# Kernel tuning notes

Measured on AMD Instinct MI355X. Metric: run time of the kernel, lower is better.

Reference implementation:

```python
import jax, jax.numpy as jnp
import numpy as np

DT = 0.1  # Euler timestep (init kwarg)

def setup_inputs() -> dict:
    key = jax.random.key(0)
    ks = jax.random.split(key, 6)
    B, L, S, U, H = 1024, 512, 64, 32, 512
    return {
        "initial_state": jax.random.normal(ks[0], (B, S), dtype=jnp.float32),
        "control_inputs": jax.random.normal(ks[1], (B, L, U), dtype=jnp.float32),
        "W1": jax.random.normal(ks[2], (S + U, H), dtype=jnp.float32) * (1.0 / np.sqrt(S + U)),
        "b1": jnp.zeros((H,), dtype=jnp.float32),
        "W2": jax.random.normal(ks[3], (H, S), dtype=jnp.float32) * (1.0 / np.sqrt(H)),
        "b2": jnp.zeros((S,), dtype=jnp.float32),
    }

def reference(initial_state, control_inputs, W1, b1, W2, b2):
    # Euler integration: state_{t+1} = state_t + dt * f(state_t, u_t)
    # f is a 2-layer tanh MLP on the concatenated [state, control].
    def step(state, u):
        z = jnp.concatenate([state, u], axis=-1)        # (B, S+U)
        diff = jnp.tanh(z @ W1 + b1) @ W2 + b2          # (B, S)
        new_state = state + diff * DT
        return new_state, new_state

    u_seq = jnp.swapaxes(control_inputs, 0, 1)          # (L, B, U)
    _, states = jax.lax.scan(step, initial_state, u_seq)  # (L, B, S)
    return jnp.swapaxes(states, 0, 1)                   # (B, L, S)
```

## Files before the change

kernel.cpp:

```cpp
#include <hip/hip_runtime.h>
#include <hip/hip_fp16.h>


typedef _Float16 f16;
typedef __attribute__((ext_vector_type(2))) _Float16 f16x2;
typedef __attribute__((ext_vector_type(8))) _Float16 f16x8;
typedef __attribute__((ext_vector_type(2))) float f32x2;
typedef __attribute__((ext_vector_type(4))) float f32x4;

#define MFMA16(a, b, c) __builtin_amdgcn_mfma_f32_16x16x32_f16((a), (b), (c), 0, 0, 0)

#define BAR() do { asm volatile("s_waitcnt lgkmcnt(0)" ::: "memory"); \
                   __builtin_amdgcn_s_barrier();                      \
                   asm volatile("" ::: "memory"); } while (0)

__device__ __forceinline__ float tanh_fast(float x) {
    float t = __builtin_amdgcn_exp2f(x * 2.885390081777927f);
    float r = __builtin_amdgcn_rcpf(t + 1.0f);
    return __builtin_fmaf(-2.0f, r, 1.0f);
}

__global__ __launch_bounds__(512, 2)
void euler_kernel(const float* __restrict__ init,
                  const float* __restrict__ uin,
                  const float* __restrict__ W1,
                  const float* __restrict__ b1,
                  const float* __restrict__ W2,
                  const float* __restrict__ b2,
                  float* __restrict__ out) {
    const int L = 512, S = 64, U = 32, H = 512;
    const int tid  = threadIdx.x;
    const int lane = tid & 63;
    const int w    = tid >> 6;
    const int g    = lane >> 4;
    const int r16  = lane & 15;
    const int b0   = blockIdx.x * 16;

    __shared__ f16   zbuf[256 * 8];
    __shared__ float pbuf[8 * 256 * 4];

    f16x8 W1F[4][4];
    f16x8 W1Fu[2][4];
    #pragma unroll
    for (int kk = 0; kk < 6; ++kk)
      #pragma unroll
      for (int nf = 0; nf < 4; ++nf) {
          const int hcol = w * 64 + 32 * (nf >> 1) + 8 * (r16 >> 2) + 4 * (nf & 1) + (r16 & 3);
          #pragma unroll
          for (int j = 0; j < 8; ++j) {
              int k  = kk * 32 + g * 8 + j;
              int kr = (k < 128) ? (k & 63) : (64 + (k & 31));
              f16 v  = (f16)W1[kr * H + hcol];
              if (kk < 4) W1F[kk][nf][j] = v; else W1Fu[kk - 4][nf][j] = v;
          }
      }
    f32x4 b1v[4];
    #pragma unroll
    for (int nf = 0; nf < 4; ++nf)
        b1v[nf] = *(const f32x4*)&b1[w * 64 + 32 * (nf >> 1) + 4 * (nf & 1) + 8 * g];

    f16x8 W2F[2][4];
    #pragma unroll
    for (int a = 0; a < 2; ++a)
      #pragma unroll
      for (int nf2 = 0; nf2 < 4; ++nf2)
        #pragma unroll
        for (int j = 0; j < 8; ++j) {
            int k = w * 64 + a * 32 + g * 8 + j;
            W2F[a][nf2][j] = (f16)W2[k * S + nf2 * 16 + r16];
        }

    f32x2 b2v    = *(const f32x2*)&b2[w * 8 + g * 2];
    f32x2 stateF = *(const f32x2*)&init[(size_t)(b0 + r16) * S + w * 8 + g * 2];
    const int zci = ((w >> 2) * 64 + (w & 3) * 16 + r16) * 8 + g * 2;
    {
        f16 h0 = (f16)stateF[0], h1 = (f16)stateF[1];
        f16x2 hi2, lo2;
        hi2[0] = h0;                              hi2[1] = h1;
        lo2[0] = (f16)(stateF[0] - (float)h0);    lo2[1] = (f16)(stateF[1] - (float)h1);
        *(f16x2*)&zbuf[zci]        = hi2;
        *(f16x2*)&zbuf[zci + 1024] = lo2;
    }

    const float* uptr = uin + (size_t)(b0 + r16) * L * U + g * 8;
    f32x4 ua0 = *(const f32x4*)uptr;
    f32x4 ua1 = *(const f32x4*)(uptr + 4);
    f32x4 uacc[4];
    #pragma unroll
    for (int nf = 0; nf < 4; ++nf) uacc[nf] = b1v[nf];
    {
        f16x8 uh, ul;
        #pragma unroll
        for (int j = 0; j < 4; ++j) {
            f16 h0 = (f16)ua0[j]; uh[j] = h0;     ul[j] = (f16)(ua0[j] - (float)h0);
            f16 h1 = (f16)ua1[j]; uh[4 + j] = h1; ul[4 + j] = (f16)(ua1[j] - (float)h1);
        }
        #pragma unroll
        for (int nf = 0; nf < 4; ++nf) uacc[nf] = MFMA16(W1Fu[0][nf], uh, uacc[nf]);
        #pragma unroll
        for (int nf = 0; nf < 4; ++nf) uacc[nf] = MFMA16(W1Fu[1][nf], ul, uacc[nf]);
    }
    ua0 = *(const f32x4*)(uptr + U);
    ua1 = *(const f32x4*)(uptr + U + 4);
    BAR();

    const int pbase = ((w >> 1) * 64 + (2 * (w & 1) + (g >> 1)) * 16 + r16) * 4 + 2 * (g & 1);

    #pragma unroll 1
    for (int t = 0; t < L; ++t) {
        f16x8 zf[4];
        #pragma unroll
        for (int kk = 0; kk < 4; ++kk)
            zf[kk] = *(const f16x8*)&zbuf[(kk * 64 + lane) * 8];
        f32x4 acc1[4];
        #pragma unroll
        for (int nf = 0; nf < 4; ++nf) acc1[nf] = uacc[nf];
        #pragma unroll
        for (int kk = 0; kk < 4; ++kk)
          #pragma unroll
          for (int nf = 0; nf < 4; ++nf)
            acc1[nf] = MFMA16(W1F[kk][nf], zf[kk], acc1[nf]);
        f16x8 hb[2];
        #pragma unroll
        for (int a = 0; a < 2; ++a)
          #pragma unroll
          for (int j8 = 0; j8 < 8; ++j8)
            hb[a][j8] = (f16)tanh_fast(acc1[a * 2 + (j8 >> 2)][j8 & 3]);
        f32x4 acc2[4];
        #pragma unroll
        for (int nf2 = 0; nf2 < 4; ++nf2) acc2[nf2] = (f32x4){0.f, 0.f, 0.f, 0.f};
        #pragma unroll
        for (int a = 0; a < 2; ++a)
          #pragma unroll
          for (int nf2 = 0; nf2 < 4; ++nf2)
            acc2[nf2] = MFMA16(W2F[a][nf2], hb[a], acc2[nf2]);
        #pragma unroll
        for (int nf2 = 0; nf2 < 4; ++nf2)
            *(f32x4*)&pbuf[(w * 256 + nf2 * 64 + lane) * 4] = acc2[nf2];

        #pragma unroll
        for (int nf = 0; nf < 4; ++nf) uacc[nf] = b1v[nf];
        {
            f16x8 uh, ul;
            #pragma unroll
            for (int j = 0; j < 4; ++j) {
                f16 h0 = (f16)ua0[j]; uh[j] = h0;     ul[j] = (f16)(ua0[j] - (float)h0);
                f16 h1 = (f16)ua1[j]; uh[4 + j] = h1; ul[4 + j] = (f16)(ua1[j] - (float)h1);
            }
            #pragma unroll
            for (int nf = 0; nf < 4; ++nf) uacc[nf] = MFMA16(W1Fu[0][nf], uh, uacc[nf]);
            #pragma unroll
            for (int nf = 0; nf < 4; ++nf) uacc[nf] = MFMA16(W1Fu[1][nf], ul, uacc[nf]);
        }
        {
            int tp = (t + 2 < L) ? (t + 2) : (L - 1);
            const float* up = uptr + (size_t)tp * U;
            ua0 = *(const f32x4*)up;
            ua1 = *(const f32x4*)(up + 4);
        }
        BAR();

        f32x2 sum = (f32x2){0.f, 0.f};
        #pragma unroll
        for (int ww = 0; ww < 8; ++ww) {
            f32x2 p = *(const f32x2*)&pbuf[ww * 1024 + pbase];
            sum[0] += p[0];
            sum[1] += p[1];
        }
        float s0 = __builtin_fmaf(0.1f, sum[0] + b2v[0], stateF[0]);
        float s1 = __builtin_fmaf(0.1f, sum[1] + b2v[1], stateF[1]);
        stateF[0] = s0; stateF[1] = s1;
        *(f32x2*)&out[((size_t)(b0 + r16) * L + t) * S + w * 8 + g * 2] = stateF;
        f16 h0 = (f16)s0, h1 = (f16)s1;
        f16x2 hi2, lo2;
        hi2[0] = h0;                     hi2[1] = h1;
        lo2[0] = (f16)(s0 - (float)h0);  lo2[1] = (f16)(s1 - (float)h1);
        *(f16x2*)&zbuf[zci]        = hi2;
        *(f16x2*)&zbuf[zci + 1024] = lo2;
        BAR();
    }
}

extern "C" void kernel_launch(void* const* d_in, const int* in_sizes, int n_in,
                              void* d_out, int out_size, void* d_ws, size_t ws_size,
                              hipStream_t stream) {
    const float* init = (const float*)d_in[0];
    const float* uin  = (const float*)d_in[1];
    const float* W1   = (const float*)d_in[2];
    const float* b1   = (const float*)d_in[3];
    const float* W2   = (const float*)d_in[4];
    const float* b2   = (const float*)d_in[5];
    euler_kernel<<<dim3(64), dim3(512), 0, stream>>>(init, uin, W1, b1, W2, b2,
                                                     (float*)d_out);
}
```

Before: 639.3 us.

## Split layer-1 MFMA chains, swap layer-2 operands, move barrier before reduction

Splits the layer-1 MFMA accumulation into two independent chains (a/b) so consecutive MFMAs don't serialize on one accumulator, summing them before tanh. Swaps the layer-2 MFMA operands so the partial outputs come out transposed, giving contiguous per-thread pbuf reads. The state-to-thread mapping is remapped to match, which turns the state writes into scalar f16 stores and the output writes into strided scalar stores. The barrier moves before the pbuf reads, so the control-input MFMAs and prefetch now overlap the LDS read latency, and the reduction uses a tree sum.

```diff
diff --git a/kernel.cpp b/kernel.cpp
--- a/kernel.cpp
+++ b/kernel.cpp
@@ -3,7 +3,6 @@
 
 
 typedef _Float16 f16;
-typedef __attribute__((ext_vector_type(2))) _Float16 f16x2;
 typedef __attribute__((ext_vector_type(8))) _Float16 f16x8;
 typedef __attribute__((ext_vector_type(2))) float f32x2;
 typedef __attribute__((ext_vector_type(4))) float f32x4;
@@ -37,7 +36,7 @@
     const int b0   = blockIdx.x * 16;
 
     __shared__ f16   zbuf[256 * 8];
-    __shared__ float pbuf[8 * 256 * 4];
+    __shared__ float pbuf[8 * 1024];
 
     f16x8 W1F[4][4];
     f16x8 W1Fu[2][4];
@@ -63,23 +62,28 @@
     #pragma unroll
     for (int a = 0; a < 2; ++a)
       #pragma unroll
-      for (int nf2 = 0; nf2 < 4; ++nf2)
+      for (int ns = 0; ns < 4; ++ns)
         #pragma unroll
         for (int j = 0; j < 8; ++j) {
             int k = w * 64 + a * 32 + g * 8 + j;
-            W2F[a][nf2][j] = (f16)W2[k * S + nf2 * 16 + r16];
-        }
-
-    f32x2 b2v    = *(const f32x2*)&b2[w * 8 + g * 2];
-    f32x2 stateF = *(const f32x2*)&init[(size_t)(b0 + r16) * S + w * 8 + g * 2];
-    const int zci = ((w >> 2) * 64 + (w & 3) * 16 + r16) * 8 + g * 2;
+            W2F[a][ns][j] = (f16)W2[k * S + ns * 16 + r16];
+        }
+
+    const int l5 = lane >> 5, r = lane & 31;
+    const int sP = (w >> 1) * 16 + (r >> 1);
+    const int bP = ((w & 1) * 2 + l5) * 4 + 2 * (r & 1);
+    const float b2v = b2[sP];
+    const int zci = ((sP >> 5) * 64 + ((sP >> 3) & 3) * 16 + bP) * 8 + (sP & 7);
+
+    f32x2 stateF;
+    stateF[0] = init[(size_t)(b0 + bP) * S + sP];
+    stateF[1] = init[(size_t)(b0 + bP + 1) * S + sP];
     {
         f16 h0 = (f16)stateF[0], h1 = (f16)stateF[1];
-        f16x2 hi2, lo2;
-        hi2[0] = h0;                              hi2[1] = h1;
-        lo2[0] = (f16)(stateF[0] - (float)h0);    lo2[1] = (f16)(stateF[1] - (float)h1);
-        *(f16x2*)&zbuf[zci]        = hi2;
-        *(f16x2*)&zbuf[zci + 1024] = lo2;
+        zbuf[zci]            = h0;
+        zbuf[zci + 8]        = h1;
+        zbuf[zci + 1024]     = (f16)(stateF[0] - (float)h0);
+        zbuf[zci + 1024 + 8] = (f16)(stateF[1] - (float)h1);
     }
 
     const float* uptr = uin + (size_t)(b0 + r16) * L * U + g * 8;
@@ -104,39 +108,53 @@
     ua1 = *(const f32x4*)(uptr + U + 4);
     BAR();
 
-    const int pbase = ((w >> 1) * 64 + (2 * (w & 1) + (g >> 1)) * 16 + r16) * 4 + 2 * (g & 1);
-
     #pragma unroll 1
     for (int t = 0; t < L; ++t) {
         f16x8 zf[4];
         #pragma unroll
         for (int kk = 0; kk < 4; ++kk)
             zf[kk] = *(const f16x8*)&zbuf[(kk * 64 + lane) * 8];
-        f32x4 acc1[4];
-        #pragma unroll
-        for (int nf = 0; nf < 4; ++nf) acc1[nf] = uacc[nf];
-        #pragma unroll
-        for (int kk = 0; kk < 4; ++kk)
-          #pragma unroll
-          for (int nf = 0; nf < 4; ++nf)
-            acc1[nf] = MFMA16(W1F[kk][nf], zf[kk], acc1[nf]);
+        f32x4 acc1a[4], acc1b[4];
+        #pragma unroll
+        for (int nf = 0; nf < 4; ++nf) {
+            acc1a[nf] = uacc[nf];
+            acc1b[nf] = (f32x4){0.f, 0.f, 0.f, 0.f};
+        }
+        #pragma unroll
+        for (int nf = 0; nf < 4; ++nf) {
+            acc1a[nf] = MFMA16(W1F[0][nf], zf[0], acc1a[nf]);
+            acc1b[nf] = MFMA16(W1F[2][nf], zf[2], acc1b[nf]);
+        }
+        #pragma unroll
+        for (int nf = 0; nf < 4; ++nf) {
+            acc1a[nf] = MFMA16(W1F[1][nf], zf[1], acc1a[nf]);
+            acc1b[nf] = MFMA16(W1F[3][nf], zf[3], acc1b[nf]);
+        }
         f16x8 hb[2];
         #pragma unroll
         for (int a = 0; a < 2; ++a)
           #pragma unroll
-          for (int j8 = 0; j8 < 8; ++j8)
-            hb[a][j8] = (f16)tanh_fast(acc1[a * 2 + (j8 >> 2)][j8 & 3]);
+          for (int j8 = 0; j8 < 8; ++j8) {
+              int nf = a * 2 + (j8 >> 2), jj = j8 & 3;
+              hb[a][j8] = (f16)tanh_fast(acc1a[nf][jj] + acc1b[nf][jj]);
+          }
         f32x4 acc2[4];
         #pragma unroll
-        for (int nf2 = 0; nf2 < 4; ++nf2) acc2[nf2] = (f32x4){0.f, 0.f, 0.f, 0.f};
+        for (int ns = 0; ns < 4; ++ns) acc2[ns] = (f32x4){0.f, 0.f, 0.f, 0.f};
         #pragma unroll
         for (int a = 0; a < 2; ++a)
           #pragma unroll
-          for (int nf2 = 0; nf2 < 4; ++nf2)
-            acc2[nf2] = MFMA16(W2F[a][nf2], hb[a], acc2[nf2]);
-        #pragma unroll
-        for (int nf2 = 0; nf2 < 4; ++nf2)
-            *(f32x4*)&pbuf[(w * 256 + nf2 * 64 + lane) * 4] = acc2[nf2];
+          for (int ns = 0; ns < 4; ++ns)
+            acc2[ns] = MFMA16(hb[a], W2F[a][ns], acc2[ns]);
+        #pragma unroll
+        for (int ns = 0; ns < 4; ++ns)
+            *(f32x4*)&pbuf[(w * 256 + ns * 64 + lane) * 4] = acc2[ns];
+        BAR();
+
+        f32x2 p[8];
+        #pragma unroll
+        for (int ww = 0; ww < 8; ++ww)
+            p[ww] = *(const f32x2*)&pbuf[ww * 1024 + w * 128 + lane * 2];
 
         #pragma unroll
         for (int nf = 0; nf < 4; ++nf) uacc[nf] = b1v[nf];
@@ -154,29 +172,30 @@
         }
         {
             int tp = (t + 2 < L) ? (t + 2) : (L - 1);
-            const float* up = uptr + (size_t)tp * U;
-            ua0 = *(const f32x4*)up;
-            ua1 = *(const f32x4*)(up + 4);
-        }
-        BAR();
-
-        f32x2 sum = (f32x2){0.f, 0.f};
-        #pragma unroll
-        for (int ww = 0; ww < 8; ++ww) {
-            f32x2 p = *(const f32x2*)&pbuf[ww * 1024 + pbase];
-            sum[0] += p[0];
-            sum[1] += p[1];
-        }
-        float s0 = __builtin_fmaf(0.1f, sum[0] + b2v[0], stateF[0]);
-        float s1 = __builtin_fmaf(0.1f, sum[1] + b2v[1], stateF[1]);
-        stateF[0] = s0; stateF[1] = s1;
-        *(f32x2*)&out[((size_t)(b0 + r16) * L + t) * S + w * 8 + g * 2] = stateF;
-        f16 h0 = (f16)s0, h1 = (f16)s1;
-        f16x2 hi2, lo2;
-        hi2[0] = h0;                     hi2[1] = h1;
-        lo2[0] = (f16)(s0 - (float)h0);  lo2[1] = (f16)(s1 - (float)h1);
-        *(f16x2*)&zbuf[zci]        = hi2;
-        *(f16x2*)&zbuf[zci + 1024] = lo2;
+            ua0 = *(const f32x4*)(uptr + (size_t)tp * U);
+            ua1 = *(const f32x4*)(uptr + (size_t)tp * U + 4);
+        }
+
+        f32x2 s01 = (f32x2){0.f, 0.f}, s23 = s01, s45 = s01, s67 = s01;
+        #pragma unroll
+        for (int j = 0; j < 2; ++j) {
+            s01[j] = p[0][j] + p[1][j];
+            s23[j] = p[2][j] + p[3][j];
+            s45[j] = p[4][j] + p[5][j];
+            s67[j] = p[6][j] + p[7][j];
+        }
+        float d0 = ((s01[0] + s23[0]) + (s45[0] + s67[0])) + b2v;
+        float d1 = ((s01[1] + s23[1]) + (s45[1] + s67[1])) + b2v;
+        float sn0 = __builtin_fmaf(0.1f, d0, stateF[0]);
+        float sn1 = __builtin_fmaf(0.1f, d1, stateF[1]);
+        stateF[0] = sn0; stateF[1] = sn1;
+        f16 h0 = (f16)sn0, h1 = (f16)sn1;
+        zbuf[zci]            = h0;
+        zbuf[zci + 8]        = h1;
+        zbuf[zci + 1024]     = (f16)(sn0 - (float)h0);
+        zbuf[zci + 1024 + 8] = (f16)(sn1 - (float)h1);
+        out[((size_t)(b0 + bP) * L + t) * S + sP]     = sn0;
+        out[((size_t)(b0 + bP + 1) * L + t) * S + sP] = sn1;
         BAR();
     }
 }
```

After: 883.3 us. 1.38x slower.
